# Performance work log

Hardware: AMD Instinct MI355X
Metric: run time of the kernel (lower is better)

## Reference

```python
import jax, jax.numpy as jnp
import numpy as np

B = 16777216

def setup_inputs() -> dict:
    key = jax.random.key(0)
    k1, k2 = jax.random.split(key)
    x = jax.random.normal(k1, (B, 2), dtype=jnp.float32)
    ws = jax.random.normal(k2, (10,), dtype=jnp.float32)  # 10 scalar Linear(1,1) weights
    return {"x": x, "ws": ws}

def _step(carry, w):
    x0, x1 = carry
    nx0 = x0 - 0.1 * x1
    nx1 = 0.1 * x0 + x1 - 0.1 * x0**3 + 0.1 * (w * x1)
    return (nx0, nx1), None

def reference(x, ws):
    (x0, x1), _ = jax.lax.scan(_step, (x[:, 0], x[:, 1]), ws)
    out = (jnp.tanh(100.0 * (x1 - 0.1)) - jnp.tanh(100.0 * (x1 + 0.1)) + 2.0) / 2.0
    return out[:, None]  # [B, 1]
```

## Files before the change

kernel.cpp:

```cpp
#include <hip/hip_runtime.h>

typedef float v2f __attribute__((ext_vector_type(2)));
typedef float v4f __attribute__((ext_vector_type(4)));

__device__ __forceinline__ v2f pk_fma(v2f a, v2f b, v2f c) {
    v2f d;
    asm("v_pk_fma_f32 %0, %1, %2, %3" : "=v"(d) : "v"(a), "v"(b), "v"(c));
    return d;
}
__device__ __forceinline__ v2f pk_mul(v2f a, v2f b) {
    v2f d;
    asm("v_pk_mul_f32 %0, %1, %2" : "=v"(d) : "v"(a), "v"(b));
    return d;
}

__device__ __forceinline__ float band(float x1) {
    const float S = 2.4258257e8f;
    float t = __builtin_fabsf(x1);
    float F = __builtin_amdgcn_exp2f(288.53900817779268f * t);
    float r = __builtin_amdgcn_rcpf(fmaf(0.5f, F, S));
    return fmaf(-S, r, 1.0f);
}

__global__ void __launch_bounds__(256)
dynsys_kernel(const v4f* __restrict__ x, const float* __restrict__ ws,
              v2f* __restrict__ out, int n4) {
    const int tid    = blockIdx.x * 256 + threadIdx.x;
    const int nthr   = gridDim.x * 256;
    const int per_it = nthr * 8;

    v2f wn[10];
#pragma unroll
    for (int k = 0; k < 10; ++k) { float v = -ws[k]; wn[k] = (v2f){v, v}; }
    const v2f mone = {-1.0f, -1.0f};
    const v2f cn01 = {-0.1f, -0.1f};

    for (int base = tid; base < n4; base += per_it) {
        v4f ld[8];
#pragma unroll
        for (int k = 0; k < 8; ++k)
            ld[k] = __builtin_nontemporal_load(&x[base + k * nthr]);

#pragma unroll
        for (int k = 0; k < 8; ++k) {
            v2f a0 = {ld[k].x, ld[k].z};
            v2f a1 = {ld[k].y, ld[k].w};
#pragma unroll
            for (int s = 0; s < 10; ++s) {
                v2f na0 = pk_fma(cn01, a1, a0);
                v2f t   = pk_fma(a0, a0, mone);
                v2f u   = pk_mul(a0, t);
                v2f d   = pk_fma(wn[s], a1, u);
                a1      = pk_fma(cn01, d, a1);
                a0      = na0;
            }
            v2f r = {band(a1.x), band(a1.y)};
            __builtin_nontemporal_store(r, &out[base + k * nthr]);
        }
    }
}

extern "C" void kernel_launch(void* const* d_in, const int* in_sizes, int n_in,
                              void* d_out, int out_size, void* d_ws, size_t ws_size,
                              hipStream_t stream) {
    const v4f*  x  = (const v4f*)d_in[0];
    const float* ws = (const float*)d_in[1];
    v2f* out = (v2f*)d_out;

    int n4 = in_sizes[0] / 4;
    dynsys_kernel<<<2048, 256, 0, stream>>>(x, ws, out, n4);
}
```

Baseline: 204.0 us.

## Software-pipeline loads with 4-element-per-thread chunks and 16-byte stores

Restructures the grid-stride loop so each thread handles 4 rows per step (two adjacent v4f loads) and prefetches the next step's input while computing the current one. Output stores widen from 8 to 16 bytes. This replaces the 8-deep batched nontemporal loads with a one-step-ahead register prefetch, aiming to overlap memory latency with the 10-step recurrence using fewer live registers. It assumes npair divides evenly by the thread count and drops the nontemporal hint on loads. Each thread now reads two consecutive v4f, so adjacent lanes' loads sit 32 bytes apart rather than 16.

```diff
diff --git a/kernel.cpp b/kernel.cpp
--- a/kernel.cpp
+++ b/kernel.cpp
@@ -22,41 +22,58 @@
     return fmaf(-S, r, 1.0f);
 }
 
+__device__ __forceinline__ v4f compute4(v4f c0, v4f c1, const v2f* __restrict__ wn) {
+    const v2f mone = {-1.0f, -1.0f};
+    const v2f cn01 = {-0.1f, -0.1f};
+    v2f A0 = {c0.x, c0.z}, A1 = {c0.y, c0.w};
+    v2f B0 = {c1.x, c1.z}, B1 = {c1.y, c1.w};
+#pragma unroll
+    for (int s = 0; s < 10; ++s) {
+        v2f nA0 = pk_fma(cn01, A1, A0);
+        v2f tA  = pk_fma(A0, A0, mone);
+        v2f uA  = pk_mul(A0, tA);
+        v2f dA  = pk_fma(wn[s], A1, uA);
+        A1      = pk_fma(cn01, dA, A1);
+        A0      = nA0;
+
+        v2f nB0 = pk_fma(cn01, B1, B0);
+        v2f tB  = pk_fma(B0, B0, mone);
+        v2f uB  = pk_mul(B0, tB);
+        v2f dB  = pk_fma(wn[s], B1, uB);
+        B1      = pk_fma(cn01, dB, B1);
+        B0      = nB0;
+    }
+    v4f r = {band(A1.x), band(A1.y), band(B1.x), band(B1.y)};
+    return r;
+}
+
 __global__ void __launch_bounds__(256)
 dynsys_kernel(const v4f* __restrict__ x, const float* __restrict__ ws,
-              v2f* __restrict__ out, int n4) {
-    const int tid    = blockIdx.x * 256 + threadIdx.x;
-    const int nthr   = gridDim.x * 256;
-    const int per_it = nthr * 8;
+              v4f* __restrict__ out, int npair) {
+    const int tid  = blockIdx.x * 256 + threadIdx.x;
+    const int nthr = gridDim.x * 256;
+    const int steps = npair / nthr;
 
     v2f wn[10];
 #pragma unroll
     for (int k = 0; k < 10; ++k) { float v = -ws[k]; wn[k] = (v2f){v, v}; }
-    const v2f mone = {-1.0f, -1.0f};
-    const v2f cn01 = {-0.1f, -0.1f};
 
-    for (int base = tid; base < n4; base += per_it) {
-        v4f ld[8];
-#pragma unroll
-        for (int k = 0; k < 8; ++k)
-            ld[k] = __builtin_nontemporal_load(&x[base + k * nthr]);
+    v4f c0 = x[2 * tid];
+    v4f c1 = x[2 * tid + 1];
 
-#pragma unroll
-        for (int k = 0; k < 8; ++k) {
-            v2f a0 = {ld[k].x, ld[k].z};
-            v2f a1 = {ld[k].y, ld[k].w};
-#pragma unroll
-            for (int s = 0; s < 10; ++s) {
-                v2f na0 = pk_fma(cn01, a1, a0);
-                v2f t   = pk_fma(a0, a0, mone);
-                v2f u   = pk_mul(a0, t);
-                v2f d   = pk_fma(wn[s], a1, u);
-                a1      = pk_fma(cn01, d, a1);
-                a0      = na0;
-            }
-            v2f r = {band(a1.x), band(a1.y)};
-            __builtin_nontemporal_store(r, &out[base + k * nthr]);
-        }
+    for (int s = 0; s < steps - 1; ++s) {
+        int p  = s * nthr + tid;
+        int pn = p + nthr;
+        v4f n0 = x[2 * pn];
+        v4f n1 = x[2 * pn + 1];
+        v4f r  = compute4(c0, c1, wn);
+        __builtin_nontemporal_store(r, &out[p]);
+        c0 = n0; c1 = n1;
+    }
+    {
+        int p = (steps - 1) * nthr + tid;
+        v4f r = compute4(c0, c1, wn);
+        __builtin_nontemporal_store(r, &out[p]);
     }
 }
 
@@ -65,8 +82,8 @@
                               hipStream_t stream) {
     const v4f*  x  = (const v4f*)d_in[0];
     const float* ws = (const float*)d_in[1];
-    v2f* out = (v2f*)d_out;
+    v4f* out = (v4f*)d_out;
 
-    int n4 = in_sizes[0] / 4;
-    dynsys_kernel<<<2048, 256, 0, stream>>>(x, ws, out, n4);
+    int npair = in_sizes[0] / 8;
+    dynsys_kernel<<<2048, 256, 0, stream>>>(x, ws, out, npair);
 }
```

New measurement: 208.4 us. +2.1%, slower.
